# Performance work log

Measured on AMD Instinct MI355X. Metric: run time of the kernel, lower is better.

Reference implementation:

```python
import jax, jax.numpy as jnp
import numpy as np

N_NODES = 100000
N_GRAPHS = 256
N_EDGES = 800000


def gcn_conv(x, W, b, src, dst):
    """PyG GCNConv: self-loops + symmetric deg^-1/2 normalization + scatter-add."""
    h = x @ W  # [N, F_out]
    # degree on graph with self-loops (edge weight 1)
    deg = jax.ops.segment_sum(jnp.ones((src.shape[0],), h.dtype), dst,
                              num_segments=N_NODES) + 1.0
    dinv = jax.lax.rsqrt(deg)  # deg^-1/2, deg >= 1 so finite
    norm = dinv[src] * dinv[dst]  # [E]
    msg = h[src] * norm[:, None]  # gather + scale, [E, F_out]
    agg = jax.ops.segment_sum(msg, dst, num_segments=N_NODES)
    # self-loop contribution: dinv[i]^2 * h[i]
    agg = agg + h * (dinv * dinv)[:, None]
    return agg + b


def setup_inputs() -> dict:
    key = jax.random.key(0)
    ks = jax.random.split(key, 16)
    inp = {
        "x": jax.random.normal(ks[0], (N_NODES, 114), jnp.float32),
        "edge_index": jax.random.randint(ks[1], (2, N_EDGES), 0, N_NODES, jnp.int64)
        if jax.config.jax_enable_x64 else jax.random.randint(ks[1], (2, N_EDGES), 0, N_NODES, jnp.int32),
        "batch": jnp.sort(jax.random.randint(ks[2], (N_NODES,), 0, N_GRAPHS,
                                             jnp.int32)),
        "W1": jax.random.normal(ks[3], (114, 230), jnp.float32) * 0.09,
        "b1": jax.random.normal(ks[4], (230,), jnp.float32) * 0.01,
        "W2": jax.random.normal(ks[5], (230, 115), jnp.float32) * 0.07,
        "b2": jax.random.normal(ks[6], (115,), jnp.float32) * 0.01,
        "Wg": jax.random.normal(ks[7], (115, 64), jnp.float32) * 0.09,
        "bg": jax.random.normal(ks[8], (64,), jnp.float32) * 0.01,
        "Wf": jax.random.normal(ks[9], (64, 32), jnp.float32) * 0.12,
        "bf": jax.random.normal(ks[10], (32,), jnp.float32) * 0.01,
        "Wo": jax.random.normal(ks[11], (32, 1), jnp.float32) * 0.17,
        "bo": jax.random.normal(ks[12], (1,), jnp.float32) * 0.01,
    }
    return inp


def reference(x, edge_index, batch, W1, b1, W2, b2, Wg, bg, Wf, bf, Wo, bo):
    src, dst = edge_index[0], edge_index[1]
    h = jax.nn.relu(gcn_conv(x, W1, b1, src, dst))
    # dropout p=0.2 is identity at inference (training=False)
    h = jax.nn.relu(gcn_conv(h, W2, b2, src, dst))
    # global max pool over graphs; h >= 0 after relu so clamp empty segments to 0
    pooled = jax.ops.segment_max(h, batch, num_segments=N_GRAPHS)
    pooled = jnp.maximum(pooled, 0.0)  # [G, 115]
    g = jax.nn.relu(pooled @ Wg + bg)
    g = jax.nn.relu(g @ Wf + bf)
    return g @ Wo + bo  # [G, 1]
```

## Files before the change

kernel.cpp:

```cpp
#include <hip/hip_runtime.h>
#include <hip/hip_bf16.h>
#include <hip/hip_fp16.h>

#define NN 100000
#define NG 256
#define NE 800000

constexpr int F0 = 114;
constexpr int F1 = 230;
constexpr int F2 = 115;
constexpr int MPAD = 100096;

typedef _Float16 __attribute__((ext_vector_type(8))) f16x8;
typedef __attribute__((ext_vector_type(4))) float f32x4;
typedef __attribute__((ext_vector_type(8))) unsigned short u16x8;

__device__ __forceinline__ unsigned short f2h_bits(float x) {
  _Float16 h = (_Float16)x;
  return __builtin_bit_cast(unsigned short, h);
}
__device__ __forceinline__ float h_bits2f(unsigned short u) {
  return (float)__builtin_bit_cast(_Float16, u);
}


__global__ void k_count(const int* __restrict__ dst, int* __restrict__ cnt) {
  int e = blockIdx.x * blockDim.x + threadIdx.x;
  if (e < NE) atomicAdd(&cnt[dst[e]], 1);
}

constexpr int SCAN_T = 256;
constexpr int SCAN_E = 1024;
constexpr int NB = (NN + SCAN_E - 1) / SCAN_E;

__global__ void k_scan1(const int* __restrict__ cnt, int* __restrict__ off,
                        int* __restrict__ bsum, float* __restrict__ dinv) {
  __shared__ int s[SCAN_T];
  int b = blockIdx.x, t = threadIdx.x;
  int base = b * SCAN_E + t * 4;
  int v0 = 0, v1 = 0, v2 = 0, v3 = 0;
  if (base + 0 < NN) v0 = cnt[base + 0];
  if (base + 1 < NN) v1 = cnt[base + 1];
  if (base + 2 < NN) v2 = cnt[base + 2];
  if (base + 3 < NN) v3 = cnt[base + 3];
  if (base + 0 < NN) dinv[base + 0] = rsqrtf((float)v0 + 1.0f);
  if (base + 1 < NN) dinv[base + 1] = rsqrtf((float)v1 + 1.0f);
  if (base + 2 < NN) dinv[base + 2] = rsqrtf((float)v2 + 1.0f);
  if (base + 3 < NN) dinv[base + 3] = rsqrtf((float)v3 + 1.0f);
  int sum = v0 + v1 + v2 + v3;
  s[t] = sum;
  __syncthreads();
  for (int ofs = 1; ofs < SCAN_T; ofs <<= 1) {
    int x = (t >= ofs) ? s[t - ofs] : 0;
    __syncthreads();
    s[t] += x;
    __syncthreads();
  }
  int excl = s[t] - sum;
  if (base + 0 < NN) off[base + 0] = excl;
  if (base + 1 < NN) off[base + 1] = excl + v0;
  if (base + 2 < NN) off[base + 2] = excl + v0 + v1;
  if (base + 3 < NN) off[base + 3] = excl + v0 + v1 + v2;
  if (t == SCAN_T - 1) bsum[b] = s[t];
}

__global__ void k_scan2(int* bsum) {
  __shared__ int ws[2];
  int t = threadIdx.x;
  int v = (t < NB) ? bsum[t] : 0;
  int orig = v;
  for (int o = 1; o < 64; o <<= 1) {
    int x = __shfl_up(v, o, 64);
    if ((t & 63) >= o) v += x;
  }
  if ((t & 63) == 63) ws[t >> 6] = v;
  __syncthreads();
  if (t >= 64) v += ws[0];
  if (t < NB) bsum[t] = v - orig;
}

__global__ void k_scan3(int* __restrict__ off, const int* __restrict__ bsum,
                        int* __restrict__ cur) {
  int i = blockIdx.x * blockDim.x + threadIdx.x;
  if (i < NN) {
    int v = off[i] + bsum[i / SCAN_E];
    off[i] = v;
    cur[i] = v;
  }
  if (i == NN) off[NN] = NE;
}

__global__ void k_place(const int* __restrict__ src, const int* __restrict__ dst,
                        int* __restrict__ cur, int* __restrict__ srcs) {
  int e = blockIdx.x * blockDim.x + threadIdx.x;
  if (e >= NE) return;
  int p = atomicAdd(&cur[dst[e]], 1);
  srcs[p] = src[e];
}


__global__ void k_prepx(const float* __restrict__ x, const float* __restrict__ dinv,
                        unsigned short* __restrict__ xd) {
  int n = blockIdx.x, f = threadIdx.x;
  float v = (f < F0) ? x[(size_t)n * F0 + f] * dinv[n] : 0.0f;
  xd[(size_t)n * 128 + f] = f2h_bits(v);
}


template <bool POOL>
__global__ __launch_bounds__(256) void k_gatherw(
    const unsigned short* __restrict__ tab, const float* __restrict__ dinv,
    const int* __restrict__ off, const int* __restrict__ srcs,
    const float* __restrict__ b2, const int* __restrict__ batch,
    unsigned short* __restrict__ outh, float* __restrict__ pooled) {
  __shared__ float smax[4][128];
  __shared__ int sg[4];
  int w = threadIdx.x >> 6, lane = threadIdx.x & 63;
  int n = blockIdx.x * 4 + w;
  int grp = lane >> 4, sub = lane & 15;
  int fb = sub * 8;

  float acc[8] = {0.f, 0.f, 0.f, 0.f, 0.f, 0.f, 0.f, 0.f};
  int j0 = off[n], j1 = off[n + 1];
  for (int base = j0; base <= j1; base += 16) {
    int row[4];
    u16x8 v[4];
    bool has[4];
#pragma unroll
    for (int c = 0; c < 4; ++c) {
      int je = base + c * 4 + grp;
      row[c] = (je < j1) ? srcs[je] : ((je == j1) ? n : -1);
      has[c] = row[c] >= 0;
    }
#pragma unroll
    for (int c = 0; c < 4; ++c)
      if (has[c]) v[c] = *(const u16x8*)&tab[(size_t)row[c] * 128 + fb];
#pragma unroll
    for (int c = 0; c < 4; ++c)
      if (has[c]) {
#pragma unroll
        for (int u = 0; u < 8; ++u) acc[u] += h_bits2f(v[c][u]);
      }
  }
#pragma unroll
  for (int u = 0; u < 8; ++u) {
    acc[u] += __shfl_xor(acc[u], 16);
    acc[u] += __shfl_xor(acc[u], 32);
  }
  float dn = dinv[n];

  if constexpr (!POOL) {
    if (grp == 0) {
      u16x8 o;
#pragma unroll
      for (int u = 0; u < 8; ++u) o[u] = f2h_bits(acc[u] * dn);
      *(u16x8*)&outh[(size_t)n * 128 + fb] = o;
    }
  } else {
    if (grp == 0) {
#pragma unroll
      for (int u = 0; u < 8; ++u) {
        int f = fb + u;
        float bb = (f < F2) ? b2[f] : 0.0f;
        smax[w][f] = fmaxf(acc[u] * dn + bb, 0.0f);
      }
      if (sub == 0) sg[w] = batch[n];
    }
    __syncthreads();
    int t = threadIdx.x;
    if (t < 128) {
      int g0 = sg[0];
      bool same = (sg[1] == g0) & (sg[2] == g0) & (sg[3] == g0);
      if (same) {
        float m = fmaxf(fmaxf(smax[0][t], smax[1][t]),
                        fmaxf(smax[2][t], smax[3][t]));
        if (t < F2 && m > 0.0f)
          atomicMax((int*)&pooled[g0 * F2 + t], __float_as_int(m));
      } else {
        for (int ww = 0; ww < 4; ++ww) {
          float m = smax[ww][t];
          if (t < F2 && m > 0.0f)
            atomicMax((int*)&pooled[sg[ww] * F2 + t], __float_as_int(m));
        }
      }
    }
  }
}


__global__ void k_prepB2(const float* __restrict__ W1, const float* __restrict__ W2,
                         unsigned short* __restrict__ B1h, unsigned short* __restrict__ B1l,
                         unsigned short* __restrict__ B2h, unsigned short* __restrict__ B2l) {
  int b = blockIdx.x, t = threadIdx.x;
  if (b < 128) {
    int n = b * 2 + (t >> 7), k = t & 127;
    float v = (k < F0 && n < F1) ? W1[(size_t)k * F1 + n] : 0.0f;
    unsigned short h = f2h_bits(v);
    unsigned short l = f2h_bits(v - h_bits2f(h));
    B1h[(size_t)n * 128 + k] = h;
    B1l[(size_t)n * 128 + k] = l;
  } else {
    int n = b - 128, k = t;
    float v = (k < F1 && n < F2) ? W2[(size_t)k * F2 + n] : 0.0f;
    unsigned short h = f2h_bits(v);
    unsigned short l = f2h_bits(v - h_bits2f(h));
    B2h[(size_t)n * 256 + k] = h;
    B2l[(size_t)n * 256 + k] = l;
  }
}


__global__ __launch_bounds__(256) void k_fused(
    const unsigned short* __restrict__ A,
    const unsigned short* __restrict__ B1h, const unsigned short* __restrict__ B1l,
    const unsigned short* __restrict__ B2h, const unsigned short* __restrict__ B2l,
    const float* __restrict__ b1, const float* __restrict__ dscale,
    unsigned short* __restrict__ td) {
  __shared__ char lds[73728];
  char* h1B = lds;
  char* AsB = lds + 32768;
  char* Bs0 = lds + 40960;
  char* Bs1 = lds + 57344;

  const int t = threadIdx.x;
  const int m0 = blockIdx.x * 64;
  const int lane = t & 63, w = t >> 6;
  const int r = lane & 15;
  const int kq = lane >> 4;
  const int kb16 = kq * 16;
  const int rq = kq * 4;
  const int wc = w * 32;
  const int swr = (r & 7) << 4;
  const int arow = t >> 2, aq = t & 3, aswz = (arow & 7) << 4;
  const int brow = t >> 1, bseg = t & 1, bswz = (brow & 7) << 4;

  f32x4 acc2[4][2];
#pragma unroll
  for (int i = 0; i < 4; ++i)
#pragma unroll
    for (int j = 0; j < 2; ++j) acc2[i][j] = (f32x4){0.f, 0.f, 0.f, 0.f};

  for (int h = 0; h < 2; ++h) {
    f32x4 acc[4][2];
#pragma unroll
    for (int i = 0; i < 4; ++i)
#pragma unroll
      for (int j = 0; j < 2; ++j) acc[i][j] = (f32x4){0.f, 0.f, 0.f, 0.f};

    for (int kc = 0; kc < 2; ++kc) {
      __syncthreads();
      {
        size_t ga = (size_t)(m0 + arow) * 128 + kc * 64 + aq * 16;
        *(u16x8*)(AsB + arow * 128 + ((aq * 32) ^ aswz))      = *(const u16x8*)&A[ga];
        *(u16x8*)(AsB + arow * 128 + ((aq * 32 + 16) ^ aswz)) = *(const u16x8*)&A[ga + 8];
        size_t gb = (size_t)(h * 128 + brow) * 128 + kc * 64 + bseg * 32;
#pragma unroll
        for (int v = 0; v < 4; ++v) {
          const int bo = (bseg * 64 + v * 16) ^ bswz;
          *(u16x8*)(Bs0 + brow * 128 + bo) = *(const u16x8*)&B1h[gb + v * 8];
          *(u16x8*)(Bs1 + brow * 128 + bo) = *(const u16x8*)&B1l[gb + v * 8];
        }
      }
      __syncthreads();
#pragma unroll
      for (int ks = 0; ks < 2; ++ks) {
        f16x8 av[4], bh[2], bl[2];
#pragma unroll
        for (int i = 0; i < 4; ++i)
          av[i] = *(const f16x8*)(AsB + (i * 16 + r) * 128 + ((ks * 64 + kb16) ^ swr));
#pragma unroll
        for (int j = 0; j < 2; ++j) {
          const int row = wc + j * 16 + r;
          const int bo = (ks * 64 + kb16) ^ swr;
          bh[j] = *(const f16x8*)(Bs0 + row * 128 + bo);
          bl[j] = *(const f16x8*)(Bs1 + row * 128 + bo);
        }
#pragma unroll
        for (int i = 0; i < 4; ++i)
#pragma unroll
          for (int j = 0; j < 2; ++j)
            acc[i][j] = __builtin_amdgcn_mfma_f32_16x16x32_f16(av[i], bl[j], acc[i][j], 0, 0, 0);
#pragma unroll
        for (int i = 0; i < 4; ++i)
#pragma unroll
          for (int j = 0; j < 2; ++j)
            acc[i][j] = __builtin_amdgcn_mfma_f32_16x16x32_f16(av[i], bh[j], acc[i][j], 0, 0, 0);
      }
    }

#pragma unroll
    for (int i = 0; i < 4; ++i)
#pragma unroll
      for (int j = 0; j < 2; ++j) {
        const int nl = wc + j * 16 + r;
        const int n = h * 128 + nl;
        const bool val = n < F1;
        const float bb = val ? b1[n] : 0.0f;
#pragma unroll
        for (int q = 0; q < 4; ++q) {
          const int ml = i * 16 + rq + q;
          const float v = val ? fmaxf(acc[i][j][q] + bb, 0.0f) : 0.0f;
          *(unsigned short*)(h1B + ml * 512 + ((n * 2) ^ ((ml & 7) << 4))) = f2h_bits(v);
        }
      }
  }

  for (int kc = 0; kc < 4; ++kc) {
    __syncthreads();
    {
      size_t gb = (size_t)brow * 256 + kc * 64 + bseg * 32;
#pragma unroll
      for (int v = 0; v < 4; ++v) {
        const int bo = (bseg * 64 + v * 16) ^ bswz;
        *(u16x8*)(Bs0 + brow * 128 + bo) = *(const u16x8*)&B2h[gb + v * 8];
        *(u16x8*)(Bs1 + brow * 128 + bo) = *(const u16x8*)&B2l[gb + v * 8];
      }
    }
    __syncthreads();
#pragma unroll
    for (int ks = 0; ks < 2; ++ks) {
      f16x8 ah[4], bh[2], bl[2];
#pragma unroll
      for (int i = 0; i < 4; ++i) {
        const int row = i * 16 + r;
        ah[i] = *(const f16x8*)(h1B + row * 512 + ((kc * 128 + ks * 64 + kb16) ^ swr));
      }
#pragma unroll
      for (int j = 0; j < 2; ++j) {
        const int row = wc + j * 16 + r;
        const int bo = (ks * 64 + kb16) ^ swr;
        bh[j] = *(const f16x8*)(Bs0 + row * 128 + bo);
        bl[j] = *(const f16x8*)(Bs1 + row * 128 + bo);
      }
#pragma unroll
      for (int i = 0; i < 4; ++i)
#pragma unroll
        for (int j = 0; j < 2; ++j)
          acc2[i][j] = __builtin_amdgcn_mfma_f32_16x16x32_f16(ah[i], bl[j], acc2[i][j], 0, 0, 0);
#pragma unroll
      for (int i = 0; i < 4; ++i)
#pragma unroll
        for (int j = 0; j < 2; ++j)
          acc2[i][j] = __builtin_amdgcn_mfma_f32_16x16x32_f16(ah[i], bh[j], acc2[i][j], 0, 0, 0);
    }
  }

  __syncthreads();
#pragma unroll
  for (int i = 0; i < 4; ++i)
#pragma unroll
    for (int j = 0; j < 2; ++j) {
      const int nl = wc + j * 16 + r;
#pragma unroll
      for (int q = 0; q < 4; ++q) {
        const int ml = i * 16 + rq + q;
        const float v = acc2[i][j][q] * dscale[m0 + ml];
        *(unsigned short*)(h1B + ml * 512 + ((nl * 2) ^ ((ml & 7) << 4))) = f2h_bits(v);
      }
    }
  __syncthreads();
  {
    const int row = t >> 2, seg = t & 3;
    const int swz = (row & 7) << 4;
    const size_t dst = (size_t)(m0 + row) * 128 + seg * 32;
#pragma unroll
    for (int v = 0; v < 4; ++v) {
      u16x8 d = *(const u16x8*)(h1B + row * 512 + ((seg * 64 + v * 16) ^ swz));
      *(u16x8*)&td[dst + v * 8] = d;
    }
  }
}


__global__ void k_mlp(const float* __restrict__ pooled,
                      const float* __restrict__ Wg, const float* __restrict__ bg,
                      const float* __restrict__ Wf, const float* __restrict__ bf,
                      const float* __restrict__ Wo, const float* __restrict__ bo,
                      float* __restrict__ out) {
  __shared__ float sp[F2];
  __shared__ float sg[64];
  __shared__ float sf[32];
  int g = blockIdx.x, t = threadIdx.x;
  for (int f = t; f < F2; f += 64) sp[f] = pooled[g * F2 + f];
  __syncthreads();
  float a = bg[t];
  for (int k = 0; k < F2; ++k) a += sp[k] * Wg[k * 64 + t];
  sg[t] = fmaxf(a, 0.0f);
  __syncthreads();
  if (t < 32) {
    float c = bf[t];
    for (int k = 0; k < 64; ++k) c += sg[k] * Wf[k * 32 + t];
    sf[t] = fmaxf(c, 0.0f);
  }
  __syncthreads();
  if (t == 0) {
    float c = bo[0];
    for (int k = 0; k < 32; ++k) c += sf[k] * Wo[k];
    out[g] = c;
  }
}


extern "C" void kernel_launch(void* const* d_in, const int* in_sizes, int n_in,
                              void* d_out, int out_size, void* d_ws, size_t ws_size,
                              hipStream_t stream) {
  const float* x  = (const float*)d_in[0];
  const int* ei   = (const int*)d_in[1];
  const int* batch = (const int*)d_in[2];
  const float* W1 = (const float*)d_in[3];
  const float* b1 = (const float*)d_in[4];
  const float* W2 = (const float*)d_in[5];
  const float* b2 = (const float*)d_in[6];
  const float* Wg = (const float*)d_in[7];
  const float* bg = (const float*)d_in[8];
  const float* Wf = (const float*)d_in[9];
  const float* bf = (const float*)d_in[10];
  const float* Wo = (const float*)d_in[11];
  const float* bo = (const float*)d_in[12];
  const int* src = ei;
  const int* dst = ei + NE;

  char* p = (char*)d_ws;
  auto alloc4 = [&](size_t units) { void* r = p; p += units * 4; return r; };
  float* dinv  = (float*)alloc4(100224);
  int* cnt     = (int*)alloc4(100224);
  int* off     = (int*)alloc4(100352);
  int* cur     = (int*)alloc4(100224);
  int* bsum    = (int*)alloc4(128);
  int* srcs    = (int*)alloc4(NE);
  unsigned short* xd   = (unsigned short*)alloc4((size_t)NN * 128 / 2);
  unsigned short* aggX = (unsigned short*)alloc4((size_t)MPAD * 128 / 2);
  unsigned short* td   = (unsigned short*)alloc4((size_t)MPAD * 128 / 2);
  unsigned short* Bt1h = (unsigned short*)alloc4(256 * 128 / 2);
  unsigned short* Bt1l = (unsigned short*)alloc4(256 * 128 / 2);
  unsigned short* Bt2h = (unsigned short*)alloc4(128 * 256 / 2);
  unsigned short* Bt2l = (unsigned short*)alloc4(128 * 256 / 2);
  float* pooled = (float*)alloc4((size_t)NG * F2);

  hipMemsetAsync(cnt, 0, 100224 * sizeof(int), stream);
  hipMemsetAsync(pooled, 0, (size_t)NG * F2 * sizeof(float), stream);

  k_count<<<(NE + 255) / 256, 256, 0, stream>>>(dst, cnt);
  k_scan1<<<NB, SCAN_T, 0, stream>>>(cnt, off, bsum, dinv);
  k_scan2<<<1, 128, 0, stream>>>(bsum);
  k_scan3<<<(NN + 256) / 256, 256, 0, stream>>>(off, bsum, cur);
  k_place<<<(NE + 255) / 256, 256, 0, stream>>>(src, dst, cur, srcs);

  k_prepB2<<<256, 256, 0, stream>>>(W1, W2, Bt1h, Bt1l, Bt2h, Bt2l);

  k_prepx<<<NN, 128, 0, stream>>>(x, dinv, xd);
  k_gatherw<false><<<NN / 4, 256, 0, stream>>>(xd, dinv, off, srcs,
                                               nullptr, nullptr, aggX, nullptr);

  k_fused<<<MPAD / 64, 256, 0, stream>>>(aggX, Bt1h, Bt1l, Bt2h, Bt2l,
                                         b1, dinv, td);

  k_gatherw<true><<<NN / 4, 256, 0, stream>>>(td, dinv, off, srcs,
                                              b2, batch, nullptr, pooled);

  k_mlp<<<NG, 64, 0, stream>>>(pooled, Wg, bg, Wf, bf, Wo, bo, (float*)d_out);
}
```

Measured before the change: 304.1 us.

## Fuse first-layer neighbor gather into the fused GEMM kernel

```diff
diff --git a/kernel.cpp b/kernel.cpp
--- a/kernel.cpp
+++ b/kernel.cpp
@@ -107,12 +107,11 @@
 }
 
 
-template <bool POOL>
 __global__ __launch_bounds__(256) void k_gatherw(
     const unsigned short* __restrict__ tab, const float* __restrict__ dinv,
     const int* __restrict__ off, const int* __restrict__ srcs,
     const float* __restrict__ b2, const int* __restrict__ batch,
-    unsigned short* __restrict__ outh, float* __restrict__ pooled) {
+    float* __restrict__ pooled) {
   __shared__ float smax[4][128];
   __shared__ int sg[4];
   int w = threadIdx.x >> 6, lane = threadIdx.x & 63;
@@ -149,39 +148,30 @@
   }
   float dn = dinv[n];
 
-  if constexpr (!POOL) {
-    if (grp == 0) {
-      u16x8 o;
-#pragma unroll
-      for (int u = 0; u < 8; ++u) o[u] = f2h_bits(acc[u] * dn);
-      *(u16x8*)&outh[(size_t)n * 128 + fb] = o;
-    }
-  } else {
-    if (grp == 0) {
-#pragma unroll
-      for (int u = 0; u < 8; ++u) {
-        int f = fb + u;
-        float bb = (f < F2) ? b2[f] : 0.0f;
-        smax[w][f] = fmaxf(acc[u] * dn + bb, 0.0f);
-      }
-      if (sub == 0) sg[w] = batch[n];
-    }
-    __syncthreads();
-    int t = threadIdx.x;
-    if (t < 128) {
-      int g0 = sg[0];
-      bool same = (sg[1] == g0) & (sg[2] == g0) & (sg[3] == g0);
-      if (same) {
-        float m = fmaxf(fmaxf(smax[0][t], smax[1][t]),
-                        fmaxf(smax[2][t], smax[3][t]));
+  if (grp == 0) {
+#pragma unroll
+    for (int u = 0; u < 8; ++u) {
+      int f = fb + u;
+      float bb = (f < F2) ? b2[f] : 0.0f;
+      smax[w][f] = fmaxf(acc[u] * dn + bb, 0.0f);
+    }
+    if (sub == 0) sg[w] = batch[n];
+  }
+  __syncthreads();
+  int t = threadIdx.x;
+  if (t < 128) {
+    int g0 = sg[0];
+    bool same = (sg[1] == g0) & (sg[2] == g0) & (sg[3] == g0);
+    if (same) {
+      float m = fmaxf(fmaxf(smax[0][t], smax[1][t]),
+                      fmaxf(smax[2][t], smax[3][t]));
+      if (t < F2 && m > 0.0f)
+        atomicMax((int*)&pooled[g0 * F2 + t], __float_as_int(m));
+    } else {
+      for (int ww = 0; ww < 4; ++ww) {
+        float m = smax[ww][t];
         if (t < F2 && m > 0.0f)
-          atomicMax((int*)&pooled[g0 * F2 + t], __float_as_int(m));
-      } else {
-        for (int ww = 0; ww < 4; ++ww) {
-          float m = smax[ww][t];
-          if (t < F2 && m > 0.0f)
-            atomicMax((int*)&pooled[sg[ww] * F2 + t], __float_as_int(m));
-        }
+          atomicMax((int*)&pooled[sg[ww] * F2 + t], __float_as_int(m));
       }
     }
   }
@@ -210,17 +200,18 @@
 }
 
 
-__global__ __launch_bounds__(256) void k_fused(
-    const unsigned short* __restrict__ A,
+__global__ __launch_bounds__(256) void k_mega(
+    const unsigned short* __restrict__ xd, const float* __restrict__ dinv,
+    const int* __restrict__ off, const int* __restrict__ srcs,
     const unsigned short* __restrict__ B1h, const unsigned short* __restrict__ B1l,
     const unsigned short* __restrict__ B2h, const unsigned short* __restrict__ B2l,
-    const float* __restrict__ b1, const float* __restrict__ dscale,
+    const float* __restrict__ b1,
     unsigned short* __restrict__ td) {
-  __shared__ char lds[73728];
+  __shared__ char lds[81920];
   char* h1B = lds;
   char* AsB = lds + 32768;
-  char* Bs0 = lds + 40960;
-  char* Bs1 = lds + 57344;
+  char* Bs0 = lds + 49152;
+  char* Bs1 = lds + 65536;
 
   const int t = threadIdx.x;
   const int m0 = blockIdx.x * 64;
@@ -231,14 +222,53 @@
   const int rq = kq * 4;
   const int wc = w * 32;
   const int swr = (r & 7) << 4;
-  const int arow = t >> 2, aq = t & 3, aswz = (arow & 7) << 4;
+  const int grp = kq, sub = r;
+  const int fb = sub * 8;
   const int brow = t >> 1, bseg = t & 1, bswz = (brow & 7) << 4;
 
-  f32x4 acc2[4][2];
-#pragma unroll
-  for (int i = 0; i < 4; ++i)
-#pragma unroll
-    for (int j = 0; j < 2; ++j) acc2[i][j] = (f32x4){0.f, 0.f, 0.f, 0.f};
+  for (int i = 0; i < 16; ++i) {
+    const int row = w * 16 + i;
+    const int n = m0 + row;
+    float acc[8] = {0.f, 0.f, 0.f, 0.f, 0.f, 0.f, 0.f, 0.f};
+    if (n < NN) {
+      const int j0 = off[n], j1 = off[n + 1];
+      for (int base = j0; base <= j1; base += 16) {
+        int rw[4];
+        u16x8 v[4];
+        bool has[4];
+#pragma unroll
+        for (int c = 0; c < 4; ++c) {
+          int je = base + c * 4 + grp;
+          rw[c] = (je < j1) ? srcs[je] : ((je == j1) ? n : -1);
+          has[c] = rw[c] >= 0;
+        }
+#pragma unroll
+        for (int c = 0; c < 4; ++c)
+          if (has[c]) v[c] = *(const u16x8*)&xd[(size_t)rw[c] * 128 + fb];
+#pragma unroll
+        for (int c = 0; c < 4; ++c)
+          if (has[c]) {
+#pragma unroll
+            for (int u = 0; u < 8; ++u) acc[u] += h_bits2f(v[c][u]);
+          }
+      }
+#pragma unroll
+      for (int u = 0; u < 8; ++u) {
+        acc[u] += __shfl_xor(acc[u], 16);
+        acc[u] += __shfl_xor(acc[u], 32);
+      }
+      const float dn = dinv[n];
+#pragma unroll
+      for (int u = 0; u < 8; ++u) acc[u] *= dn;
+    }
+    if (grp == 0) {
+      u16x8 o;
+#pragma unroll
+      for (int u = 0; u < 8; ++u) o[u] = f2h_bits(acc[u]);
+      *(u16x8*)(AsB + row * 256 + ((sub * 16) ^ ((row & 7) << 4))) = o;
+    }
+  }
+  __syncthreads();
 
   for (int h = 0; h < 2; ++h) {
     f32x4 acc[4][2];
@@ -248,11 +278,8 @@
       for (int j = 0; j < 2; ++j) acc[i][j] = (f32x4){0.f, 0.f, 0.f, 0.f};
 
     for (int kc = 0; kc < 2; ++kc) {
-      __syncthreads();
+      if (h | kc) __syncthreads();
       {
-        size_t ga = (size_t)(m0 + arow) * 128 + kc * 64 + aq * 16;
-        *(u16x8*)(AsB + arow * 128 + ((aq * 32) ^ aswz))      = *(const u16x8*)&A[ga];
-        *(u16x8*)(AsB + arow * 128 + ((aq * 32 + 16) ^ aswz)) = *(const u16x8*)&A[ga + 8];
         size_t gb = (size_t)(h * 128 + brow) * 128 + kc * 64 + bseg * 32;
 #pragma unroll
         for (int v = 0; v < 4; ++v) {
@@ -267,7 +294,8 @@
         f16x8 av[4], bh[2], bl[2];
 #pragma unroll
         for (int i = 0; i < 4; ++i)
-          av[i] = *(const f16x8*)(AsB + (i * 16 + r) * 128 + ((ks * 64 + kb16) ^ swr));
+          av[i] = *(const f16x8*)(AsB + (i * 16 + r) * 256 +
+                                  ((kc * 128 + ks * 64 + kb16) ^ swr));
 #pragma unroll
         for (int j = 0; j < 2; ++j) {
           const int row = wc + j * 16 + r;
@@ -305,6 +333,12 @@
       }
   }
 
+  f32x4 acc2[4][2];
+#pragma unroll
+  for (int i = 0; i < 4; ++i)
+#pragma unroll
+    for (int j = 0; j < 2; ++j) acc2[i][j] = (f32x4){0.f, 0.f, 0.f, 0.f};
+
   for (int kc = 0; kc < 4; ++kc) {
     __syncthreads();
     {
@@ -354,7 +388,9 @@
 #pragma unroll
       for (int q = 0; q < 4; ++q) {
         const int ml = i * 16 + rq + q;
-        const float v = acc2[i][j][q] * dscale[m0 + ml];
+        const int m = m0 + ml;
+        const float ds = (m < NN) ? dinv[m] : 0.0f;
+        const float v = acc2[i][j][q] * ds;
         *(unsigned short*)(h1B + ml * 512 + ((nl * 2) ^ ((ml & 7) << 4))) = f2h_bits(v);
       }
     }
@@ -429,7 +465,6 @@
   int* bsum    = (int*)alloc4(128);
   int* srcs    = (int*)alloc4(NE);
   unsigned short* xd   = (unsigned short*)alloc4((size_t)NN * 128 / 2);
-  unsigned short* aggX = (unsigned short*)alloc4((size_t)MPAD * 128 / 2);
   unsigned short* td   = (unsigned short*)alloc4((size_t)MPAD * 128 / 2);
   unsigned short* Bt1h = (unsigned short*)alloc4(256 * 128 / 2);
   unsigned short* Bt1l = (unsigned short*)alloc4(256 * 128 / 2);
@@ -449,14 +484,11 @@
   k_prepB2<<<256, 256, 0, stream>>>(W1, W2, Bt1h, Bt1l, Bt2h, Bt2l);
 
   k_prepx<<<NN, 128, 0, stream>>>(x, dinv, xd);
-  k_gatherw<false><<<NN / 4, 256, 0, stream>>>(xd, dinv, off, srcs,
-                                               nullptr, nullptr, aggX, nullptr);
-
-  k_fused<<<MPAD / 64, 256, 0, stream>>>(aggX, Bt1h, Bt1l, Bt2h, Bt2l,
-                                         b1, dinv, td);
-
-  k_gatherw<true><<<NN / 4, 256, 0, stream>>>(td, dinv, off, srcs,
-                                              b2, batch, nullptr, pooled);
+
+  k_mega<<<MPAD / 64, 256, 0, stream>>>(xd, dinv, off, srcs,
+                                        Bt1h, Bt1l, Bt2h, Bt2l, b1, td);
+
+  k_gatherw<<<NN / 4, 256, 0, stream>>>(td, dinv, off, srcs, b2, batch, pooled);
 
   k_mlp<<<NG, 64, 0, stream>>>(pooled, Wg, bg, Wf, bf, Wo, bo, (float*)d_out);
 }
```

Measured after the change: 371.5 us. 22.1% more time.

## Prefetch weight tiles into registers and load A tile once in fused GEMM

Applied to the files above, without the earlier changes.

```diff
diff --git a/kernel.cpp b/kernel.cpp
--- a/kernel.cpp
+++ b/kernel.cpp
@@ -216,11 +216,11 @@
     const unsigned short* __restrict__ B2h, const unsigned short* __restrict__ B2l,
     const float* __restrict__ b1, const float* __restrict__ dscale,
     unsigned short* __restrict__ td) {
-  __shared__ char lds[73728];
+  __shared__ char lds[81920];
   char* h1B = lds;
   char* AsB = lds + 32768;
-  char* Bs0 = lds + 40960;
-  char* Bs1 = lds + 57344;
+  char* Bs0 = lds + 49152;
+  char* Bs1 = lds + 65536;
 
   const int t = threadIdx.x;
   const int m0 = blockIdx.x * 64;
@@ -231,43 +231,69 @@
   const int rq = kq * 4;
   const int wc = w * 32;
   const int swr = (r & 7) << 4;
-  const int arow = t >> 2, aq = t & 3, aswz = (arow & 7) << 4;
+  const int arow = t >> 2, aseg = t & 3, aswz = (arow & 7) << 4;
   const int brow = t >> 1, bseg = t & 1, bswz = (brow & 7) << 4;
 
-  f32x4 acc2[4][2];
+  {
+    size_t ga = (size_t)(m0 + arow) * 128 + aseg * 32;
+#pragma unroll
+    for (int v = 0; v < 4; ++v) {
+      u16x8 d = *(const u16x8*)&A[ga + v * 8];
+      *(u16x8*)(AsB + arow * 256 + ((aseg * 64 + v * 16) ^ aswz)) = d;
+    }
+  }
+  u16x8 ph[4], pl[4];
+  {
+    size_t gb = (size_t)brow * 128 + bseg * 32;
+#pragma unroll
+    for (int v = 0; v < 4; ++v) {
+      ph[v] = *(const u16x8*)&B1h[gb + v * 8];
+      pl[v] = *(const u16x8*)&B1l[gb + v * 8];
+    }
+  }
+
+  f32x4 acc1[4][2], acc2[4][2];
 #pragma unroll
   for (int i = 0; i < 4; ++i)
 #pragma unroll
-    for (int j = 0; j < 2; ++j) acc2[i][j] = (f32x4){0.f, 0.f, 0.f, 0.f};
-
-  for (int h = 0; h < 2; ++h) {
-    f32x4 acc[4][2];
-#pragma unroll
-    for (int i = 0; i < 4; ++i)
-#pragma unroll
-      for (int j = 0; j < 2; ++j) acc[i][j] = (f32x4){0.f, 0.f, 0.f, 0.f};
-
-    for (int kc = 0; kc < 2; ++kc) {
-      __syncthreads();
-      {
-        size_t ga = (size_t)(m0 + arow) * 128 + kc * 64 + aq * 16;
-        *(u16x8*)(AsB + arow * 128 + ((aq * 32) ^ aswz))      = *(const u16x8*)&A[ga];
-        *(u16x8*)(AsB + arow * 128 + ((aq * 32 + 16) ^ aswz)) = *(const u16x8*)&A[ga + 8];
-        size_t gb = (size_t)(h * 128 + brow) * 128 + kc * 64 + bseg * 32;
-#pragma unroll
-        for (int v = 0; v < 4; ++v) {
-          const int bo = (bseg * 64 + v * 16) ^ bswz;
-          *(u16x8*)(Bs0 + brow * 128 + bo) = *(const u16x8*)&B1h[gb + v * 8];
-          *(u16x8*)(Bs1 + brow * 128 + bo) = *(const u16x8*)&B1l[gb + v * 8];
-        }
-      }
-      __syncthreads();
+    for (int j = 0; j < 2; ++j) {
+      acc1[i][j] = (f32x4){0.f, 0.f, 0.f, 0.f};
+      acc2[i][j] = (f32x4){0.f, 0.f, 0.f, 0.f};
+    }
+
+#pragma unroll
+  for (int rd = 0; rd < 8; ++rd) {
+    __syncthreads();
+#pragma unroll
+    for (int v = 0; v < 4; ++v) {
+      const int bo = (bseg * 64 + v * 16) ^ bswz;
+      *(u16x8*)(Bs0 + brow * 128 + bo) = ph[v];
+      *(u16x8*)(Bs1 + brow * 128 + bo) = pl[v];
+    }
+    if (rd < 7) {
+      const int nr = rd + 1;
+      const unsigned short* Gh = (nr < 4) ? B1h : B2h;
+      const unsigned short* Gl = (nr < 4) ? B1l : B2l;
+      const size_t gb = (nr < 4)
+          ? (size_t)((nr >> 1) * 128 + brow) * 128 + (nr & 1) * 64 + bseg * 32
+          : (size_t)brow * 256 + (nr - 4) * 64 + bseg * 32;
+#pragma unroll
+      for (int v = 0; v < 4; ++v) {
+        ph[v] = *(const u16x8*)&Gh[gb + v * 8];
+        pl[v] = *(const u16x8*)&Gl[gb + v * 8];
+      }
+    }
+    __syncthreads();
+
+    if (rd < 4) {
+      const int kc = rd & 1;
 #pragma unroll
       for (int ks = 0; ks < 2; ++ks) {
         f16x8 av[4], bh[2], bl[2];
 #pragma unroll
         for (int i = 0; i < 4; ++i)
-          av[i] = *(const f16x8*)(AsB + (i * 16 + r) * 128 + ((ks * 64 + kb16) ^ swr));
+          av[i] = *(const f16x8*)(AsB + (i * 16 + r) * 256 +
+                                  ((kc * 128 + ks * 64 + kb16) ^ swr));
 #pragma unroll
         for (int j = 0; j < 2; ++j) {
           const int row = wc + j * 16 + r;
@@ -279,69 +305,63 @@
         for (int i = 0; i < 4; ++i)
 #pragma unroll
           for (int j = 0; j < 2; ++j)
-            acc[i][j] = __builtin_amdgcn_mfma_f32_16x16x32_f16(av[i], bl[j], acc[i][j], 0, 0, 0);
+            acc1[i][j] = __builtin_amdgcn_mfma_f32_16x16x32_f16(av[i], bl[j], acc1[i][j], 0, 0, 0);
 #pragma unroll
         for (int i = 0; i < 4; ++i)
 #pragma unroll
           for (int j = 0; j < 2; ++j)
-            acc[i][j] = __builtin_amdgcn_mfma_f32_16x16x32_f16(av[i], bh[j], acc[i][j], 0, 0, 0);
-      }
-    }
-
-#pragma unroll
-    for (int i = 0; i < 4; ++i)
-#pragma unroll
-      for (int j = 0; j < 2; ++j) {
-        const int nl = wc + j * 16 + r;
-        const int n = h * 128 + nl;
-        const bool val = n < F1;
-        const float bb = val ? b1[n] : 0.0f;
-#pragma unroll
-        for (int q = 0; q < 4; ++q) {
-          const int ml = i * 16 + rq + q;
-          const float v = val ? fmaxf(acc[i][j][q] + bb, 0.0f) : 0.0f;
-          *(unsigned short*)(h1B + ml * 512 + ((n * 2) ^ ((ml & 7) << 4))) = f2h_bits(v);
+            acc1[i][j] = __builtin_amdgcn_mfma_f32_16x16x32_f16(av[i], bh[j], acc1[i][j], 0, 0, 0);
+      }
+      if (rd == 1 || rd == 3) {
+        const int h = rd >> 1;
+#pragma unroll
+        for (int i = 0; i < 4; ++i)
+#pragma unroll
+          for (int j = 0; j < 2; ++j) {
+            const int nl = wc + j * 16 + r;
+            const int n = h * 128 + nl;
+            const bool val = n < F1;
+            const float bb = val ? b1[n] : 0.0f;
+#pragma unroll
+            for (int q = 0; q < 4; ++q) {
+              const int ml = i * 16 + rq + q;
+              const float v = val ? fmaxf(acc1[i][j][q] + bb, 0.0f) : 0.0f;
+              *(unsigned short*)(h1B + ml * 512 + ((n * 2) ^ ((ml & 7) << 4))) = f2h_bits(v);
+            }
+          }
+#pragma unroll
+        for (int i = 0; i < 4; ++i)
+#pragma unroll
+          for (int j = 0; j < 2; ++j) acc1[i][j] = (f32x4){0.f, 0.f, 0.f, 0.f};
+      }
+    } else {
+      const int kc = rd - 4;
+#pragma unroll
+      for (int ks = 0; ks < 2; ++ks) {
+        f16x8 ah[4], bh[2], bl[2];
+#pragma unroll
+        for (int i = 0; i < 4; ++i) {
+          const int row = i * 16 + r;
+          ah[i] = *(const f16x8*)(h1B + row * 512 + ((kc * 128 + ks * 64 + kb16) ^ swr));
         }
-      }
-  }
-
-  for (int kc = 0; kc < 4; ++kc) {
-    __syncthreads();
-    {
-      size_t gb = (size_t)brow * 256 + kc * 64 + bseg * 32;
-#pragma unroll
-      for (int v = 0; v < 4; ++v) {
-        const int bo = (bseg * 64 + v * 16) ^ bswz;
-        *(u16x8*)(Bs0 + brow * 128 + bo) = *(const u16x8*)&B2h[gb + v * 8];
-        *(u16x8*)(Bs1 + brow * 128 + bo) = *(const u16x8*)&B2l[gb + v * 8];
-      }
-    }
-    __syncthreads();
-#pragma unroll
-    for (int ks = 0; ks < 2; ++ks) {
-      f16x8 ah[4], bh[2], bl[2];
-#pragma unroll
-      for (int i = 0; i < 4; ++i) {
-        const int row = i * 16 + r;
-        ah[i] = *(const f16x8*)(h1B + row * 512 + ((kc * 128 + ks * 64 + kb16) ^ swr));
-      }
-#pragma unroll
-      for (int j = 0; j < 2; ++j) {
-        const int row = wc + j * 16 + r;
-        const int bo = (ks * 64 + kb16) ^ swr;
-        bh[j] = *(const f16x8*)(Bs0 + row * 128 + bo);
-        bl[j] = *(const f16x8*)(Bs1 + row * 128 + bo);
-      }
-#pragma unroll
-      for (int i = 0; i < 4; ++i)
-#pragma unroll
-        for (int j = 0; j < 2; ++j)
-          acc2[i][j] = __builtin_amdgcn_mfma_f32_16x16x32_f16(ah[i], bl[j], acc2[i][j], 0, 0, 0);
-#pragma unroll
-      for (int i = 0; i < 4; ++i)
-#pragma unroll
-        for (int j = 0; j < 2; ++j)
-          acc2[i][j] = __builtin_amdgcn_mfma_f32_16x16x32_f16(ah[i], bh[j], acc2[i][j], 0, 0, 0);
+#pragma unroll
+        for (int j = 0; j < 2; ++j) {
+          const int row = wc + j * 16 + r;
+          const int bo = (ks * 64 + kb16) ^ swr;
+          bh[j] = *(const f16x8*)(Bs0 + row * 128 + bo);
+          bl[j] = *(const f16x8*)(Bs1 + row * 128 + bo);
+        }
+#pragma unroll
+        for (int i = 0; i < 4; ++i)
+#pragma unroll
+          for (int j = 0; j < 2; ++j)
+            acc2[i][j] = __builtin_amdgcn_mfma_f32_16x16x32_f16(ah[i], bl[j], acc2[i][j], 0, 0, 0);
+#pragma unroll
+        for (int i = 0; i < 4; ++i)
+#pragma unroll
+          for (int j = 0; j < 2; ++j)
+            acc2[i][j] = __builtin_amdgcn_mfma_f32_16x16x32_f16(ah[i], bh[j], acc2[i][j], 0, 0, 0);
+      }
     }
   }
 
```

New measurement: 302.4 us. About the same (-0.6%).
